# Optimization experiments

Measured on AMD Instinct MI355X. Metric: run time of the kernel, lower is better.

Reference implementation:

```python
import jax, jax.numpy as jnp
import numpy as np

B, T, M, L, NMEL, DSPK = 32, 512, 2048, 1024, 80, 256
MEL_LW, DUR_W, SPK_W, DIA_LW, DIAR = 1.0, 1.0, 1.0, 0.1, 8.0


def setup_inputs() -> dict:
    key = jax.random.key(0)
    ks = jax.random.split(key, 12)
    x_lengths = jax.random.randint(ks[0], (B,), T // 2, T + 1)
    lip_length = jax.random.randint(ks[1], (B,), L // 2, L + 1)
    mel_lens = jax.random.randint(ks[2], (B,), M // 2, M + 1)
    # True = padded position (same convention as the torch module)
    src_masks = jnp.arange(T)[None, :] >= x_lengths[:, None]
    lip_masks = jnp.arange(L)[None, :] >= lip_length[:, None]
    mel_masks = jnp.arange(M)[None, :] >= mel_lens[:, None]
    return {
        'texts': jax.random.randint(ks[3], (B, T), 0, 100),
        'speaker_targets': jax.random.randint(ks[3], (B,), 0, 100),
        'mel_targets': jax.random.normal(ks[4], (B, M, NMEL), jnp.float32),
        'pitch_targets': jax.random.normal(ks[5], (B, T), jnp.float32),
        'energy_targets': jax.random.normal(ks[5], (B, T), jnp.float32),
        'mel_lens': mel_lens,
        'duration_targets': jax.random.randint(ks[6], (B, T), 1, 16),
        'ref_linguistic_targets': jax.random.randint(ks[6], (B, T), 0, 100),
        'mel_predictions': jax.random.normal(ks[7], (B, M, NMEL), jnp.float32),
        'postnet_mel_predictions': jax.random.normal(ks[8], (B, M, NMEL), jnp.float32),
        'log_duration_predictions': jax.random.normal(ks[9], (B, T), jnp.float32),
        'src_masks': src_masks,
        'mel_masks': mel_masks,
        'ref_mel_masks': mel_masks,
        'speaker_predicts': jax.random.normal(ks[10], (B, DSPK), jnp.float32),
        'spk_embedding': jax.random.normal(ks[11], (B, DSPK), jnp.float32),
        'attn_scores': jax.random.uniform(ks[11], (B, T, L), jnp.float32, 1e-3, 1.0),
        'x_lengths': x_lengths,
        'lip_length': lip_length,
        'lip_masks': lip_masks,
    }


def reference(texts, speaker_targets, mel_targets, pitch_targets, energy_targets,
              mel_lens, duration_targets, ref_linguistic_targets, mel_predictions,
              postnet_mel_predictions, log_duration_predictions, src_masks, mel_masks,
              ref_mel_masks, speaker_predicts, spk_embedding, attn_scores, x_lengths,
              lip_length, lip_masks):
    dtype = mel_targets.dtype
    # ---- diagonal constraint on attention [B, L, T] ----
    attn = jnp.swapaxes(attn_scores, 1, 2)  # [B, L, T]
    attn_ks = lip_length.astype(jnp.float32) / x_lengths.astype(jnp.float32)  # [B]
    da = lip_length.astype(jnp.float32) / DIAR                                 # [B]
    tt = jnp.arange(attn.shape[2], dtype=jnp.float32)                          # [T]
    y1 = jnp.floor(attn_ks[:, None] * tt[None, :] + da[:, None])               # [B,T]
    y2 = jnp.floor(jnp.maximum(attn_ks[:, None] * tt[None, :] - da[:, None], 0.0))
    rows = jnp.arange(attn.shape[1], dtype=jnp.float32)                        # [L]
    valid_t = tt[None, :] < x_lengths[:, None].astype(jnp.float32)             # [B,T]
    diag = ((rows[None, :, None] >= y2[:, None, :])
            & (rows[None, :, None] < y1[:, None, :])
            & valid_t[:, None, :]).astype(dtype)                               # [B,L,T]
    attn = attn * (1.0 - src_masks.astype(dtype))[:, None, :]
    attn = attn * (1.0 - lip_masks.astype(dtype))[:, :, None]
    focus = (attn * diag).sum((-1, -2)) / attn.sum((-1, -2))                   # [B]
    diagonal_loss = DIA_LW * -jnp.log(focus.mean())
    # ---- masked mel MAE (masked_select mean == masked sum / count) ----
    mm = (~mel_masks).astype(dtype)[:, :, None]           # [B,M,1], True=valid
    cnt = mm.sum() * mel_targets.shape[-1]
    mel_loss = MEL_LW * (jnp.abs(mel_predictions - mel_targets) * mm).sum() / cnt
    postnet_mel_loss = MEL_LW * (jnp.abs(postnet_mel_predictions - mel_targets) * mm).sum() / cnt
    # ---- masked duration MSE in log domain ----
    sm = (~src_masks).astype(jnp.float32)                 # [B,T]
    log_dur_t = jnp.log(duration_targets.astype(jnp.float32) + 1.0)
    duration_loss = DUR_W * (((log_duration_predictions - log_dur_t) ** 2) * sm).sum() / sm.sum()
    # ---- speaker cosine loss (torch F.cosine_similarity with eps) ----
    eps = 1e-6
    num = (speaker_predicts * spk_embedding).sum(-1)
    n1 = jnp.sqrt((speaker_predicts ** 2).sum(-1))
    n2 = jnp.sqrt((spk_embedding ** 2).sum(-1))
    cos = num / (jnp.maximum(n1, eps) * jnp.maximum(n2, eps))
    speaker_loss = SPK_W * (1.0 - cos).mean()
    total_loss = mel_loss + postnet_mel_loss + duration_loss + speaker_loss + diagonal_loss
    return (total_loss, mel_loss, postnet_mel_loss, speaker_loss, duration_loss, diagonal_loss)
```

## Files before the change

kernel.cpp:

```cpp
#include <hip/hip_runtime.h>
#include <math.h>

#define B_    32
#define T_    512
#define M_    2048
#define L_    1024
#define NMEL_ 80
#define DSPK_ 256

#define NB_MEL  512
#define NB_ATTN 1024
#define NB_DUR  8
#define NB_SPK  32
#define NB_TOT  (NB_MEL + NB_ATTN + NB_DUR + NB_SPK)

#define WS_ATTN (NB_MEL * 2)
#define WS_DUR  (WS_ATTN + NB_ATTN * 2)
#define WS_SPK  (WS_DUR + NB_DUR)

__device__ __forceinline__ void red2(float& a, float& b) {
    __shared__ float la[4], lb[4];
    #pragma unroll
    for (int off = 32; off > 0; off >>= 1) {
        a += __shfl_down(a, off);
        b += __shfl_down(b, off);
    }
    int lane = threadIdx.x & 63, w = threadIdx.x >> 6;
    if (lane == 0) { la[w] = a; lb[w] = b; }
    __syncthreads();
    if (threadIdx.x == 0) {
        a = la[0] + la[1] + la[2] + la[3];
        b = lb[0] + lb[1] + lb[2] + lb[3];
    }
}

__device__ __forceinline__ void red3(float& a, float& b, float& c) {
    __shared__ float la[4], lb[4], lc[4];
    #pragma unroll
    for (int off = 32; off > 0; off >>= 1) {
        a += __shfl_down(a, off);
        b += __shfl_down(b, off);
        c += __shfl_down(c, off);
    }
    int lane = threadIdx.x & 63, w = threadIdx.x >> 6;
    if (lane == 0) { la[w] = a; lb[w] = b; lc[w] = c; }
    __syncthreads();
    if (threadIdx.x == 0) {
        a = la[0] + la[1] + la[2] + la[3];
        b = lb[0] + lb[1] + lb[2] + lb[3];
        c = lc[0] + lc[1] + lc[2] + lc[3];
    }
}

__device__ __forceinline__ float mae4(float4 p, float4 t) {
    return fabsf(p.x - t.x) + fabsf(p.y - t.y) + fabsf(p.z - t.z) + fabsf(p.w - t.w);
}

__device__ __forceinline__ void attn_row(float4 v, int t, float ks, float da,
                                         int l0, float m0, float m1, float m2, float m3,
                                         float& s1, float& s2) {
    float tf = (float)t;
    float y1f = floorf(__fadd_rn(__fmul_rn(ks, tf), da));
    float y2f = floorf(fmaxf(__fsub_rn(__fmul_rn(ks, tf), da), 0.0f));
    int y1i = (int)y1f, y2i = (int)y2f;
    float w0 = v.x * m0, w1 = v.y * m1, w2 = v.z * m2, w3 = v.w * m3;
    s1 += w0 + w1 + w2 + w3;
    s2 += ((l0 + 0 >= y2i) && (l0 + 0 < y1i)) ? w0 : 0.0f;
    s2 += ((l0 + 1 >= y2i) && (l0 + 1 < y1i)) ? w1 : 0.0f;
    s2 += ((l0 + 2 >= y2i) && (l0 + 2 < y1i)) ? w2 : 0.0f;
    s2 += ((l0 + 3 >= y2i) && (l0 + 3 < y1i)) ? w3 : 0.0f;
}

__global__ __launch_bounds__(256) void fused_kernel(
    const float* __restrict__ mel_t, const float* __restrict__ mel_p,
    const float* __restrict__ post_p, const int* __restrict__ mel_lens,
    const float* __restrict__ attn, const int* __restrict__ xl_,
    const int* __restrict__ ll_, const int* __restrict__ dur_t,
    const float* __restrict__ ldp, const float* __restrict__ spk_p,
    const float* __restrict__ spk_e, float* __restrict__ ws) {
    int blk = blockIdx.x, tid = threadIdx.x;

    if (blk < NB_MEL) {
        int b = blk >> 4, chunk = blk & 15;
        int r0 = chunk << 7;
        int ml = mel_lens[b]; if (ml > M_) ml = M_;
        int rv = ml - r0; if (rv < 0) rv = 0; if (rv > 128) rv = 128;
        int n4 = rv * (NMEL_ / 4);
        const float4* t4 = (const float4*)mel_t + (size_t)(b * M_ + r0) * (NMEL_ / 4);
        const float4* p4 = (const float4*)mel_p + (size_t)(b * M_ + r0) * (NMEL_ / 4);
        const float4* q4 = (const float4*)post_p + (size_t)(b * M_ + r0) * (NMEL_ / 4);
        float s0 = 0.0f, s1 = 0.0f;
        int i = tid;
        for (; i + 256 < n4; i += 512) {
            float4 ta = t4[i],       pa = p4[i],       qa = q4[i];
            float4 tb = t4[i + 256], pb = p4[i + 256], qb = q4[i + 256];
            s0 += mae4(pa, ta) + mae4(pb, tb);
            s1 += mae4(qa, ta) + mae4(qb, tb);
        }
        if (i < n4) {
            float4 ta = t4[i], pa = p4[i], qa = q4[i];
            s0 += mae4(pa, ta);
            s1 += mae4(qa, ta);
        }
        red2(s0, s1);
        if (tid == 0) { ws[blk * 2] = s0; ws[blk * 2 + 1] = s1; }

    } else if (blk < NB_MEL + NB_ATTN) {
        int a = blk - NB_MEL;
        int b = a >> 5, chunk = a & 31;
        int t0 = chunk << 4;
        int xl = xl_[b], ll = ll_[b];
        float ks = (float)ll / (float)xl;
        float da = (float)ll * 0.125f;
        int tv = ((xl < t0 + 16) ? xl : (t0 + 16)) - t0; if (tv < 0) tv = 0;
        const float4* a4 = (const float4*)attn + ((size_t)b * T_ + t0) * (L_ / 4);
        int l0 = tid * 4;
        float m0 = (l0 + 0 < ll) ? 1.0f : 0.0f;
        float m1 = (l0 + 1 < ll) ? 1.0f : 0.0f;
        float m2 = (l0 + 2 < ll) ? 1.0f : 0.0f;
        float m3 = (l0 + 3 < ll) ? 1.0f : 0.0f;
        float s1 = 0.0f, s2 = 0.0f;
        int r = 0;
        for (; r + 1 < tv; r += 2) {
            float4 va = a4[(size_t)r * (L_ / 4) + tid];
            float4 vb = a4[(size_t)(r + 1) * (L_ / 4) + tid];
            attn_row(va, t0 + r,     ks, da, l0, m0, m1, m2, m3, s1, s2);
            attn_row(vb, t0 + r + 1, ks, da, l0, m0, m1, m2, m3, s1, s2);
        }
        if (r < tv) {
            float4 va = a4[(size_t)r * (L_ / 4) + tid];
            attn_row(va, t0 + r, ks, da, l0, m0, m1, m2, m3, s1, s2);
        }
        red2(s1, s2);
        if (tid == 0) { ws[WS_ATTN + a * 2] = s1; ws[WS_ATTN + a * 2 + 1] = s2; }

    } else if (blk < NB_MEL + NB_ATTN + NB_DUR) {
        int d = blk - (NB_MEL + NB_ATTN);
        int base = d * (B_ * T_ / NB_DUR);
        float s = 0.0f;
        #pragma unroll
        for (int k = 0; k < (B_ * T_ / NB_DUR); k += 256) {
            int i = base + k + tid;
            int b = i >> 9, t = i & (T_ - 1);
            float diff = ldp[i] - logf((float)dur_t[i] + 1.0f);
            s += (t < xl_[b]) ? diff * diff : 0.0f;
        }
        float dummy = 0.0f;
        red2(s, dummy);
        if (tid == 0) ws[WS_DUR + d] = s;

    } else {
        int b = blk - (NB_MEL + NB_ATTN + NB_DUR);
        float av = spk_p[b * DSPK_ + tid], cv = spk_e[b * DSPK_ + tid];
        float n = av * cv, x = av * av, y = cv * cv;
        red3(n, x, y);
        if (tid == 0) {
            ws[WS_SPK + 3 * b]     = n;
            ws[WS_SPK + 3 * b + 1] = x;
            ws[WS_SPK + 3 * b + 2] = y;
        }
    }
}

__global__ __launch_bounds__(256) void final_kernel(
    const int* __restrict__ mel_lens, const int* __restrict__ xl_,
    const float* __restrict__ ws, float* __restrict__ out) {
    int tid = threadIdx.x;
    __shared__ float sA[256], sB[256];
    __shared__ float perb[B_];
    __shared__ float res[4];

    float s0 = 0.0f, s1 = 0.0f;
    for (int i = tid; i < NB_MEL; i += 256) { s0 += ws[2 * i]; s1 += ws[2 * i + 1]; }
    red2(s0, s1);
    if (tid == 0) { res[0] = s0; res[1] = s1; }
    __syncthreads();

    {
        int b = tid >> 3, c0 = (tid & 7) * 4;
        float t1 = 0.0f, t2 = 0.0f;
        #pragma unroll
        for (int c = c0; c < c0 + 4; ++c) {
            int a = b * 32 + c;
            t1 += ws[WS_ATTN + 2 * a];
            t2 += ws[WS_ATTN + 2 * a + 1];
        }
        sA[tid] = t1; sB[tid] = t2;
    }
    __syncthreads();
    if (tid < B_) {
        float t1 = 0.0f, t2 = 0.0f;
        #pragma unroll
        for (int k = 0; k < 8; ++k) { t1 += sA[tid * 8 + k]; t2 += sB[tid * 8 + k]; }
        perb[tid] = t2 / t1;
    }
    __syncthreads();
    __shared__ float focus_mean, spk_mean, sm_s, cnt_s;
    if (tid == 0) {
        float f = 0.0f;
        for (int b = 0; b < B_; ++b) f += perb[b];
        focus_mean = f / (float)B_;
    }
    __syncthreads();

    if (tid < B_) {
        float n = ws[WS_SPK + 3 * tid], x = ws[WS_SPK + 3 * tid + 1], y = ws[WS_SPK + 3 * tid + 2];
        const float eps = 1e-6f;
        float cosv = n / (fmaxf(sqrtf(x), eps) * fmaxf(sqrtf(y), eps));
        perb[tid] = 1.0f - cosv;
    }
    if (tid < B_) { sA[tid] = (float)min(xl_[tid], T_); sB[tid] = (float)min(mel_lens[tid], M_); }
    __syncthreads();
    if (tid == 0) {
        float spk = 0.0f, sm = 0.0f, cnt = 0.0f;
        for (int b = 0; b < B_; ++b) { spk += perb[b]; sm += sA[b]; cnt += sB[b]; }
        spk_mean = spk / (float)B_;
        sm_s = sm;
        cnt_s = cnt * (float)NMEL_;

        float sd = 0.0f;
        for (int d = 0; d < NB_DUR; ++d) sd += ws[WS_DUR + d];

        float mel  = res[0] / cnt_s;
        float post = res[1] / cnt_s;
        float dur  = sd / sm_s;
        float dia  = 0.1f * (-logf(focus_mean));
        out[0] = mel + post + dur + spk_mean + dia;
        out[1] = mel;
        out[2] = post;
        out[3] = spk_mean;
        out[4] = dur;
        out[5] = dia;
    }
}

extern "C" void kernel_launch(void* const* d_in, const int* in_sizes, int n_in,
                              void* d_out, int out_size, void* d_ws, size_t ws_size,
                              hipStream_t stream) {
    (void)in_sizes; (void)n_in; (void)out_size; (void)ws_size;
    const float* mel_t   = (const float*)d_in[2];
    const int*   mel_len = (const int*)  d_in[5];
    const int*   dur_t   = (const int*)  d_in[6];
    const float* mel_p   = (const float*)d_in[8];
    const float* post_p  = (const float*)d_in[9];
    const float* ldp     = (const float*)d_in[10];
    const float* spk_p   = (const float*)d_in[14];
    const float* spk_e   = (const float*)d_in[15];
    const float* attn    = (const float*)d_in[16];
    const int*   xl      = (const int*)  d_in[17];
    const int*   ll      = (const int*)  d_in[18];
    float* ws  = (float*)d_ws;
    float* out = (float*)d_out;

    hipLaunchKernelGGL(fused_kernel, dim3(NB_TOT), dim3(256), 0, stream,
                       mel_t, mel_p, post_p, mel_len, attn, xl, ll,
                       dur_t, ldp, spk_p, spk_e, ws);
    hipLaunchKernelGGL(final_kernel, dim3(1), dim3(256), 0, stream,
                       mel_len, xl, ws, out);
}
```

Measured before the change: 181.3 us.

## Fuse final reduction into main kernel via last-block atomic counter; skip masked attn loads

Removes the separate single-block final kernel: each block bumps an atomic counter in the workspace after a threadfence, and the last block to finish does the cross-block reduction and writes the outputs. A memset on the counter is added before launch. Separately, attention loads for columns beyond the lip length are now skipped and replaced with zeros, which cuts memory traffic for padded columns. This trades a kernel launch for an extra memset and atomic/fence overhead in every block.

```diff
diff --git a/kernel.cpp b/kernel.cpp
--- a/kernel.cpp
+++ b/kernel.cpp
@@ -14,7 +14,8 @@
 #define NB_SPK  32
 #define NB_TOT  (NB_MEL + NB_ATTN + NB_DUR + NB_SPK)
 
-#define WS_ATTN (NB_MEL * 2)
+#define WS_MEL  16
+#define WS_ATTN (WS_MEL + NB_MEL * 2)
 #define WS_DUR  (WS_ATTN + NB_ATTN * 2)
 #define WS_SPK  (WS_DUR + NB_DUR)
 
@@ -77,7 +78,8 @@
     const float* __restrict__ attn, const int* __restrict__ xl_,
     const int* __restrict__ ll_, const int* __restrict__ dur_t,
     const float* __restrict__ ldp, const float* __restrict__ spk_p,
-    const float* __restrict__ spk_e, float* __restrict__ ws) {
+    const float* __restrict__ spk_e, float* __restrict__ ws,
+    float* __restrict__ out) {
     int blk = blockIdx.x, tid = threadIdx.x;
 
     if (blk < NB_MEL) {
@@ -103,7 +105,7 @@
             s1 += mae4(qa, ta);
         }
         red2(s0, s1);
-        if (tid == 0) { ws[blk * 2] = s0; ws[blk * 2 + 1] = s1; }
+        if (tid == 0) { ws[WS_MEL + blk * 2] = s0; ws[WS_MEL + blk * 2 + 1] = s1; }
 
     } else if (blk < NB_MEL + NB_ATTN) {
         int a = blk - NB_MEL;
@@ -115,20 +117,22 @@
         int tv = ((xl < t0 + 16) ? xl : (t0 + 16)) - t0; if (tv < 0) tv = 0;
         const float4* a4 = (const float4*)attn + ((size_t)b * T_ + t0) * (L_ / 4);
         int l0 = tid * 4;
+        bool ldok = (l0 < ll);
         float m0 = (l0 + 0 < ll) ? 1.0f : 0.0f;
         float m1 = (l0 + 1 < ll) ? 1.0f : 0.0f;
         float m2 = (l0 + 2 < ll) ? 1.0f : 0.0f;
         float m3 = (l0 + 3 < ll) ? 1.0f : 0.0f;
+        const float4 z4 = make_float4(0.0f, 0.0f, 0.0f, 0.0f);
         float s1 = 0.0f, s2 = 0.0f;
         int r = 0;
         for (; r + 1 < tv; r += 2) {
-            float4 va = a4[(size_t)r * (L_ / 4) + tid];
-            float4 vb = a4[(size_t)(r + 1) * (L_ / 4) + tid];
+            float4 va = ldok ? a4[(size_t)r * (L_ / 4) + tid] : z4;
+            float4 vb = ldok ? a4[(size_t)(r + 1) * (L_ / 4) + tid] : z4;
             attn_row(va, t0 + r,     ks, da, l0, m0, m1, m2, m3, s1, s2);
             attn_row(vb, t0 + r + 1, ks, da, l0, m0, m1, m2, m3, s1, s2);
         }
         if (r < tv) {
-            float4 va = a4[(size_t)r * (L_ / 4) + tid];
+            float4 va = ldok ? a4[(size_t)r * (L_ / 4) + tid] : z4;
             attn_row(va, t0 + r, ks, da, l0, m0, m1, m2, m3, s1, s2);
         }
         red2(s1, s2);
@@ -160,18 +164,26 @@
             ws[WS_SPK + 3 * b + 2] = y;
         }
     }
-}
-
-__global__ __launch_bounds__(256) void final_kernel(
-    const int* __restrict__ mel_lens, const int* __restrict__ xl_,
-    const float* __restrict__ ws, float* __restrict__ out) {
-    int tid = threadIdx.x;
+
+    __shared__ int is_last;
+    __threadfence();
+    if (tid == 0) {
+        int old = atomicAdd((int*)ws, 1);
+        is_last = (old == NB_TOT - 1) ? 1 : 0;
+    }
+    __syncthreads();
+    if (!is_last) return;
+    __threadfence();
+
     __shared__ float sA[256], sB[256];
     __shared__ float perb[B_];
-    __shared__ float res[4];
+    __shared__ float res[2];
 
     float s0 = 0.0f, s1 = 0.0f;
-    for (int i = tid; i < NB_MEL; i += 256) { s0 += ws[2 * i]; s1 += ws[2 * i + 1]; }
+    for (int i = tid; i < NB_MEL; i += 256) {
+        s0 += ws[WS_MEL + 2 * i];
+        s1 += ws[WS_MEL + 2 * i + 1];
+    }
     red2(s0, s1);
     if (tid == 0) { res[0] = s0; res[1] = s1; }
     __syncthreads();
@@ -195,7 +207,7 @@
         perb[tid] = t2 / t1;
     }
     __syncthreads();
-    __shared__ float focus_mean, spk_mean, sm_s, cnt_s;
+    __shared__ float focus_mean;
     if (tid == 0) {
         float f = 0.0f;
         for (int b = 0; b < B_; ++b) f += perb[b];
@@ -208,27 +220,27 @@
         const float eps = 1e-6f;
         float cosv = n / (fmaxf(sqrtf(x), eps) * fmaxf(sqrtf(y), eps));
         perb[tid] = 1.0f - cosv;
-    }
-    if (tid < B_) { sA[tid] = (float)min(xl_[tid], T_); sB[tid] = (float)min(mel_lens[tid], M_); }
+        sA[tid] = (float)min(xl_[tid], T_);
+        sB[tid] = (float)min(mel_lens[tid], M_);
+    }
     __syncthreads();
     if (tid == 0) {
         float spk = 0.0f, sm = 0.0f, cnt = 0.0f;
         for (int b = 0; b < B_; ++b) { spk += perb[b]; sm += sA[b]; cnt += sB[b]; }
-        spk_mean = spk / (float)B_;
-        sm_s = sm;
-        cnt_s = cnt * (float)NMEL_;
+        spk /= (float)B_;
+        cnt *= (float)NMEL_;
 
         float sd = 0.0f;
         for (int d = 0; d < NB_DUR; ++d) sd += ws[WS_DUR + d];
 
-        float mel  = res[0] / cnt_s;
-        float post = res[1] / cnt_s;
-        float dur  = sd / sm_s;
+        float mel  = res[0] / cnt;
+        float post = res[1] / cnt;
+        float dur  = sd / sm;
         float dia  = 0.1f * (-logf(focus_mean));
-        out[0] = mel + post + dur + spk_mean + dia;
+        out[0] = mel + post + dur + spk + dia;
         out[1] = mel;
         out[2] = post;
-        out[3] = spk_mean;
+        out[3] = spk;
         out[4] = dur;
         out[5] = dia;
     }
@@ -252,9 +264,8 @@
     float* ws  = (float*)d_ws;
     float* out = (float*)d_out;
 
+    hipMemsetAsync(d_ws, 0, 4, stream);
     hipLaunchKernelGGL(fused_kernel, dim3(NB_TOT), dim3(256), 0, stream,
                        mel_t, mel_p, post_p, mel_len, attn, xl, ll,
-                       dur_t, ldp, spk_p, spk_e, ws);
-    hipLaunchKernelGGL(final_kernel, dim3(1), dim3(256), 0, stream,
-                       mel_len, xl, ws, out);
-}
+                       dur_t, ldp, spk_p, spk_e, ws, out);
+}
```

Measured after the change: 412.8 us. 128% more time.
